# Kernel optimization log

Hardware: AMD Instinct MI355X
Metric: run time of the kernel (lower is better)

Reference implementation:

```python
import jax, jax.numpy as jnp
import numpy as np
import math

B, M, C, H = 4, 2048, 512, 8
DQK = C // 4 // H  # 16 per-head query/key dim


def setup_inputs() -> dict:
    key = jax.random.key(0)
    ks = jax.random.split(key, 8)
    s = 0.02
    return {
        "x": jax.random.normal(ks[0], (B, M, C), dtype=jnp.float32),
        "mask": jax.random.randint(ks[1], (B, M), 0, 2, dtype=jnp.int32),
        "Wq": jax.random.normal(ks[2], (C, C // 4), dtype=jnp.float32) * s,
        "bq": jnp.zeros((C // 4,), dtype=jnp.float32),
        "Wk": jax.random.normal(ks[3], (C, C // 4), dtype=jnp.float32) * s,
        "bk": jnp.zeros((C // 4,), dtype=jnp.float32),
        "Wv": jax.random.normal(ks[4], (C, C), dtype=jnp.float32) * s,
        "bv": jnp.zeros((C,), dtype=jnp.float32),
        "gamma": jnp.ones((1,), dtype=jnp.float32),
    }


def reference(x, mask, Wq, bq, Wk, bk, Wv, bv, gamma):
    b, m, c = x.shape
    # projections, split heads: q/k -> (B, H, M, DQK), v -> (B, H, M, C//H)
    q = (x @ Wq + bq).reshape(b, m, H, -1).transpose(0, 2, 1, 3)
    k = (x @ Wk + bk).reshape(b, m, H, -1).transpose(0, 2, 1, 3)
    v = (x @ Wv + bv).reshape(b, m, H, -1).transpose(0, 2, 1, 3)
    scale = 1.0 / math.sqrt(q.shape[-1])
    scores = jnp.einsum('bhmd,bhnd->bhmn', q, k) * scale
    beta = jax.nn.softmax(jax.nn.relu(scores), axis=-1)  # act='relu' pre-softmax
    # att_drop = 0.0 -> identity
    mf = mask.astype(x.dtype)[:, None, None, :]  # (B,1,1,M)
    beta = beta * mf
    beta = beta / (beta.sum(-1, keepdims=True) + 1e-12)
    o = gamma * jnp.einsum('bhmn,bhnd->bhmd', beta, v)  # (B,H,M,C//H)
    return o.transpose(0, 2, 1, 3).reshape(b, m, c)
```

## Files before the change

### kernel.cpp

```cpp
#include <hip/hip_runtime.h>
#include <hip/hip_bf16.h>

#define MSEQ 2048

typedef __attribute__((ext_vector_type(8))) short short8;
typedef __attribute__((ext_vector_type(4))) float f32x4;

static __device__ __forceinline__ short bf16b(float f) {
    __hip_bfloat16 h = __float2bfloat16(f);
    return *reinterpret_cast<short*>(&h);
}

static __device__ __forceinline__ unsigned int pk2(float a, float b) {
    float2 f2; f2.x = a; f2.y = b;
    __hip_bfloat162 p = __float22bfloat162_rn(f2);
    return *reinterpret_cast<unsigned int*>(&p);
}

static __device__ __forceinline__ void gl_lds16(const void* g, void* l) {
    __builtin_amdgcn_global_load_lds(
        (const __attribute__((address_space(1))) unsigned int*)g,
        (__attribute__((address_space(3))) unsigned int*)l, 16, 0, 0);
}

__global__ __launch_bounds__(256) void wtrans_kernel(
    const float* __restrict__ Wq, const float* __restrict__ Wk,
    const float* __restrict__ Wv, unsigned short* __restrict__ WT)
{
    const int nt = blockIdx.x;
    const int kt = blockIdx.y;
    const int t  = threadIdx.x;
    const int k0 = kt*64;

    const float* W; int ld, n0;
    if (nt < 2)      { W = Wq; ld = 128; n0 = nt*64; }
    else if (nt < 4) { W = Wk; ld = 128; n0 = (nt-2)*64; }
    else             { W = Wv; ld = 512; n0 = (nt-4)*64; }

    __shared__ unsigned short Ts[64*72];

    #pragma unroll
    for (int s = 0; s < 4; ++s) {
        const int lin = s*256 + t;
        const int krow = lin >> 4, ng = lin & 15;
        const float4 v = *(const float4*)(W + (size_t)(k0+krow)*ld + n0 + ng*4);
        Ts[(ng*4+0)*72 + krow] = (unsigned short)bf16b(v.x);
        Ts[(ng*4+1)*72 + krow] = (unsigned short)bf16b(v.y);
        Ts[(ng*4+2)*72 + krow] = (unsigned short)bf16b(v.z);
        Ts[(ng*4+3)*72 + krow] = (unsigned short)bf16b(v.w);
    }
    __syncthreads();
    #pragma unroll
    for (int s = 0; s < 2; ++s) {
        const int lin = s*256 + t;
        const int nrow = lin >> 3, kg = lin & 7;
        *(short8*)(WT + (size_t)(nt*64 + nrow)*512 + k0 + kg*8) = *(const short8*)&Ts[nrow*72 + kg*8];
    }
}

__global__ __launch_bounds__(256, 2) void proj_mfma(
    const float* __restrict__ x, const unsigned short* __restrict__ WT,
    const float* __restrict__ bq, const float* __restrict__ bk, const float* __restrict__ bv,
    unsigned short* __restrict__ Qh, unsigned short* __restrict__ Kh, unsigned short* __restrict__ Vf)
{
    const int nt = blockIdx.x;
    const int r0 = blockIdx.y * 128;
    const int n0 = nt * 128;
    const int t = threadIdx.x, w = t >> 6, lane = t & 63, l15 = lane & 15, quad = lane >> 4;
    const int wqh = w >> 1, wch = w & 1;

    __shared__ short smem[128*136];
    short* As = smem;
    short* Bs = smem + 128*32;

    f32x4 acc[4][4];
    #pragma unroll
    for (int i = 0; i < 4; ++i)
        #pragma unroll
        for (int j = 0; j < 4; ++j) acc[i][j] = {0.f,0.f,0.f,0.f};

    const int brow = lane >> 2, bkg = lane & 3;

    for (int kk = 0; kk < 512; kk += 32) {
        #pragma unroll
        for (int s = 0; s < 2; ++s)
            gl_lds16(WT + (size_t)(n0 + w*32 + s*16 + brow)*512 + kk + bkg*8,
                     Bs + (w*32 + s*16)*32);
        #pragma unroll
        for (int s = 0; s < 4; ++s) {
            const int idx = s*256 + t;
            const int row = idx >> 3, cg = idx & 7;
            const float4 v = *(const float4*)(x + (size_t)(r0+row)*512 + kk + cg*4);
            uint2 uu; uu.x = pk2(v.x, v.y); uu.y = pk2(v.z, v.w);
            *(uint2*)&As[row*32 + cg*4] = uu;
        }
        __syncthreads();
        short8 Af[4], Bf[4];
        #pragma unroll
        for (int i = 0; i < 4; ++i) Af[i] = *(const short8*)&As[(wqh*64 + i*16 + l15)*32 + quad*8];
        #pragma unroll
        for (int j = 0; j < 4; ++j) Bf[j] = *(const short8*)&Bs[(wch*64 + j*16 + l15)*32 + quad*8];
        #pragma unroll
        for (int i = 0; i < 4; ++i)
            #pragma unroll
            for (int j = 0; j < 4; ++j)
                acc[i][j] = __builtin_amdgcn_mfma_f32_16x16x32_bf16(Af[i], Bf[j], acc[i][j], 0, 0, 0);
        __syncthreads();
    }

    const float* bias = (nt == 0) ? bq : (nt == 1) ? bk : (bv + (nt-2)*128);
    float bj[4];
    #pragma unroll
    for (int j = 0; j < 4; ++j) bj[j] = bias[wch*64 + j*16 + l15];

    short* Ts = smem;
    if (nt < 2) {
        #pragma unroll
        for (int i = 0; i < 4; ++i)
            #pragma unroll
            for (int j = 0; j < 4; ++j)
                #pragma unroll
                for (int r = 0; r < 4; ++r)
                    Ts[(wqh*64 + i*16 + quad*4 + r)*136 + wch*64 + j*16 + l15] =
                        bf16b(acc[i][j][r] + bj[j]);
    } else {
        #pragma unroll
        for (int i = 0; i < 4; ++i)
            #pragma unroll
            for (int j = 0; j < 4; ++j)
                #pragma unroll
                for (int r = 0; r < 4; ++r)
                    Ts[(wch*64 + j*16 + l15)*136 + wqh*64 + i*16 + quad*4 + r] =
                        bf16b(acc[i][j][r] + bj[j]);
    }
    __syncthreads();

    const int b = r0 >> 11, key0 = r0 & 2047;
    if (nt < 2) {
        unsigned short* Out = (nt == 0) ? Qh : Kh;
        #pragma unroll
        for (int s = 0; s < 8; ++s) {
            const int lin = s*256 + t, row = lin >> 4, seg = lin & 15;
            const int h = seg >> 1, dh = seg & 1;
            *(short8*)(Out + ((size_t)(b*8 + h)*MSEQ + key0 + row)*16 + dh*8) =
                *(const short8*)&Ts[row*136 + seg*8];
        }
    } else {
        const int kt0 = key0 >> 6, h0 = (nt-2)*2;
        #pragma unroll
        for (int s = 0; s < 8; ++s) {
            const int lin = s*256 + t;
            const int lane_ = lin & 63, kh = (lin>>6)&1, ci = (lin>>7)&1;
            const int chh = (lin>>8)&1, kt_l = (lin>>9)&1, h_l = (lin>>10)&1;
            const int l15_ = lane_ & 15, quad_ = lane_ >> 4;
            const int ch_local  = h_l*64 + (chh*2+ci)*16 + l15_;
            const int key_local = kt_l*64 + kh*32 + quad_*8;
            const size_t addr = ((((((size_t)(b*8 + h0 + h_l)*32 + kt0 + kt_l)*2 + chh)*2 + ci)*2 + kh)*512)
                                + lane_*8;
            *(short8*)(Vf + addr) = *(const short8*)&Ts[ch_local*136 + key_local];
        }
    }
}

__global__ __launch_bounds__(256, 4) void attn_mfma(
    const unsigned short* __restrict__ Qh, const unsigned short* __restrict__ Kh,
    const unsigned short* __restrict__ Vf, const int* __restrict__ mask,
    const float* __restrict__ gamma, float* __restrict__ out)
{
    const int m0 = blockIdx.x * 64;
    const int bh = blockIdx.y;
    const int b  = bh >> 3, h = bh & 7;
    const int t  = threadIdx.x;
    const int wave = t >> 6, lane = t & 63, l15 = lane & 15, quad = lane >> 4;
    const int qh = wave >> 1, chh = wave & 1;

    __shared__ short Ws[2*64*68];
    __shared__ float wsl[4*64];
    __shared__ float wsums[64];

    const short8 zz = {0,0,0,0,0,0,0,0};

    const unsigned short* Qrow = Qh + (size_t)(b*8 + h)*MSEQ*16;
    const unsigned short* Krow = Kh + (size_t)(b*8 + h)*MSEQ*16;
    const unsigned short* Vbh  = Vf + (size_t)(b*8 + h)*32*4096;

    short8 qfrag[4];
    #pragma unroll
    for (int c = 0; c < 4; ++c)
        qfrag[c] = (quad < 2)
            ? *(const short8*)(Qrow + (size_t)(m0 + c*16 + l15)*16 + quad*8)
            : zz;

    f32x4 acc[2][2] = {{{0.f,0.f,0.f,0.f},{0.f,0.f,0.f,0.f}},
                       {{0.f,0.f,0.f,0.f},{0.f,0.f,0.f,0.f}}};
    float wsum_acc[4] = {0.f,0.f,0.f,0.f};

    for (int kt = 0; kt < 32; ++kt) {
        const int kn0 = kt*64;
        short* Wp = Ws + (kt & 1)*64*68;

        const short8 kfrag = (quad < 2)
            ? *(const short8*)(Krow + (size_t)(kn0 + wave*16 + l15)*16 + quad*8)
            : zz;
        const int4 mi = *(const int4*)(mask + b*MSEQ + kn0 + wave*16 + quad*4);
        const float mk[4] = {(float)mi.x, (float)mi.y, (float)mi.z, (float)mi.w};

        #pragma unroll
        for (int c = 0; c < 4; ++c) {
            f32x4 s = {0.f,0.f,0.f,0.f};
            s = __builtin_amdgcn_mfma_f32_16x16x32_bf16(kfrag, qfrag[c], s, 0, 0, 0);
            float w0 = mk[0] * __expf(fmaxf(0.25f*s[0], 0.f));
            float w1 = mk[1] * __expf(fmaxf(0.25f*s[1], 0.f));
            float w2 = mk[2] * __expf(fmaxf(0.25f*s[2], 0.f));
            float w3 = mk[3] * __expf(fmaxf(0.25f*s[3], 0.f));
            uint2 uu; uu.x = pk2(w0, w1); uu.y = pk2(w2, w3);
            *(uint2*)&Wp[(c*16 + l15)*68 + wave*16 + quad*4] = uu;
            wsum_acc[c] += (w0 + w1) + (w2 + w3);
        }

        short8 Bf[2][2];
        #pragma unroll
        for (int ci = 0; ci < 2; ++ci)
            #pragma unroll
            for (int kh = 0; kh < 2; ++kh)
                Bf[ci][kh] = *(const short8*)(Vbh
                    + (size_t)((((kt*2 + chh)*2 + ci)*2 + kh))*512 + lane*8);

        __syncthreads();

        short8 Af[2][2];
        #pragma unroll
        for (int si = 0; si < 2; ++si)
            #pragma unroll
            for (int kh = 0; kh < 2; ++kh)
                Af[si][kh] = *(const short8*)&Wp[((qh*2+si)*16 + l15)*68 + kh*32 + quad*8];
        #pragma unroll
        for (int si = 0; si < 2; ++si)
            #pragma unroll
            for (int ci = 0; ci < 2; ++ci)
                #pragma unroll
                for (int kh = 0; kh < 2; ++kh)
                    acc[si][ci] = __builtin_amdgcn_mfma_f32_16x16x32_bf16(
                        Af[si][kh], Bf[ci][kh], acc[si][ci], 0, 0, 0);
    }

    #pragma unroll
    for (int c = 0; c < 4; ++c) {
        float v = wsum_acc[c];
        v += __shfl_xor(v, 16, 64);
        v += __shfl_xor(v, 32, 64);
        if (quad == 0) wsl[wave*64 + c*16 + l15] = v;
    }
    __syncthreads();
    if (t < 64) wsums[t] = (wsl[t] + wsl[64+t]) + (wsl[128+t] + wsl[192+t]);
    __syncthreads();

    const float g = gamma[0];
    #pragma unroll
    for (int si = 0; si < 2; ++si) {
        #pragma unroll
        for (int r = 0; r < 4; ++r) {
            const int row = qh*32 + si*16 + quad*4 + r;
            const float inv = g / fmaxf(wsums[row], 1e-20f);
            #pragma unroll
            for (int ci = 0; ci < 2; ++ci) {
                const int col = chh*32 + ci*16 + l15;
                out[(size_t)(b*MSEQ + m0 + row)*512 + h*64 + col] = acc[si][ci][r] * inv;
            }
        }
    }
}

extern "C" void kernel_launch(void* const* d_in, const int* in_sizes, int n_in,
                              void* d_out, int out_size, void* d_ws, size_t ws_size,
                              hipStream_t stream) {
    const float* x     = (const float*)d_in[0];
    const int*   mask  = (const int*)  d_in[1];
    const float* Wq    = (const float*)d_in[2];
    const float* bq    = (const float*)d_in[3];
    const float* Wk    = (const float*)d_in[4];
    const float* bk    = (const float*)d_in[5];
    const float* Wv    = (const float*)d_in[6];
    const float* bv    = (const float*)d_in[7];
    const float* gamma = (const float*)d_in[8];
    float* outp = (float*)d_out;

    unsigned short* WT = (unsigned short*)d_ws;
    unsigned short* Qh = WT + (size_t)768*512;
    unsigned short* Kh = Qh + (size_t)8192*128;
    unsigned short* Vf = Kh + (size_t)8192*128;

    wtrans_kernel<<<dim3(12, 8), 256, 0, stream>>>(Wq, Wk, Wv, WT);
    proj_mfma<<<dim3(6, 64), 256, 0, stream>>>(x, WT, bq, bk, bv, Qh, Kh, Vf);
    attn_mfma<<<dim3(32, 32), 256, 0, stream>>>(Qh, Kh, Vf, mask, gamma, outp);
}
```

Measured before the change: 174.1 us.

## Halve projection row tile and prefetch next K/V/mask tiles in attention

```diff
diff --git a/kernel.cpp b/kernel.cpp
--- a/kernel.cpp
+++ b/kernel.cpp
@@ -58,24 +58,24 @@
     }
 }
 
-__global__ __launch_bounds__(256, 2) void proj_mfma(
+__global__ __launch_bounds__(256, 4) void proj_mfma(
     const float* __restrict__ x, const unsigned short* __restrict__ WT,
     const float* __restrict__ bq, const float* __restrict__ bk, const float* __restrict__ bv,
     unsigned short* __restrict__ Qh, unsigned short* __restrict__ Kh, unsigned short* __restrict__ Vf)
 {
     const int nt = blockIdx.x;
-    const int r0 = blockIdx.y * 128;
+    const int r0 = blockIdx.y * 64;
     const int n0 = nt * 128;
     const int t = threadIdx.x, w = t >> 6, lane = t & 63, l15 = lane & 15, quad = lane >> 4;
     const int wqh = w >> 1, wch = w & 1;
 
-    __shared__ short smem[128*136];
+    __shared__ short smem[128*72];
     short* As = smem;
-    short* Bs = smem + 128*32;
-
-    f32x4 acc[4][4];
-    #pragma unroll
-    for (int i = 0; i < 4; ++i)
+    short* Bs = smem + 64*32;
+
+    f32x4 acc[2][4];
+    #pragma unroll
+    for (int i = 0; i < 2; ++i)
         #pragma unroll
         for (int j = 0; j < 4; ++j) acc[i][j] = {0.f,0.f,0.f,0.f};
 
@@ -87,7 +87,7 @@
             gl_lds16(WT + (size_t)(n0 + w*32 + s*16 + brow)*512 + kk + bkg*8,
                      Bs + (w*32 + s*16)*32);
         #pragma unroll
-        for (int s = 0; s < 4; ++s) {
+        for (int s = 0; s < 2; ++s) {
             const int idx = s*256 + t;
             const int row = idx >> 3, cg = idx & 7;
             const float4 v = *(const float4*)(x + (size_t)(r0+row)*512 + kk + cg*4);
@@ -95,13 +95,13 @@
             *(uint2*)&As[row*32 + cg*4] = uu;
         }
         __syncthreads();
-        short8 Af[4], Bf[4];
-        #pragma unroll
-        for (int i = 0; i < 4; ++i) Af[i] = *(const short8*)&As[(wqh*64 + i*16 + l15)*32 + quad*8];
+        short8 Af[2], Bf[4];
+        #pragma unroll
+        for (int i = 0; i < 2; ++i) Af[i] = *(const short8*)&As[(wqh*32 + i*16 + l15)*32 + quad*8];
         #pragma unroll
         for (int j = 0; j < 4; ++j) Bf[j] = *(const short8*)&Bs[(wch*64 + j*16 + l15)*32 + quad*8];
         #pragma unroll
-        for (int i = 0; i < 4; ++i)
+        for (int i = 0; i < 2; ++i)
             #pragma unroll
             for (int j = 0; j < 4; ++j)
                 acc[i][j] = __builtin_amdgcn_mfma_f32_16x16x32_bf16(Af[i], Bf[j], acc[i][j], 0, 0, 0);
@@ -113,51 +113,49 @@
     #pragma unroll
     for (int j = 0; j < 4; ++j) bj[j] = bias[wch*64 + j*16 + l15];
 
-    short* Ts = smem;
+    const int b = r0 >> 11, key0 = r0 & 2047;
     if (nt < 2) {
-        #pragma unroll
-        for (int i = 0; i < 4; ++i)
+        short* Ts = smem;
+        #pragma unroll
+        for (int i = 0; i < 2; ++i)
             #pragma unroll
             for (int j = 0; j < 4; ++j)
                 #pragma unroll
                 for (int r = 0; r < 4; ++r)
-                    Ts[(wqh*64 + i*16 + quad*4 + r)*136 + wch*64 + j*16 + l15] =
+                    Ts[(wqh*32 + i*16 + quad*4 + r)*136 + wch*64 + j*16 + l15] =
                         bf16b(acc[i][j][r] + bj[j]);
-    } else {
-        #pragma unroll
-        for (int i = 0; i < 4; ++i)
-            #pragma unroll
-            for (int j = 0; j < 4; ++j)
-                #pragma unroll
-                for (int r = 0; r < 4; ++r)
-                    Ts[(wch*64 + j*16 + l15)*136 + wqh*64 + i*16 + quad*4 + r] =
-                        bf16b(acc[i][j][r] + bj[j]);
-    }
-    __syncthreads();
-
-    const int b = r0 >> 11, key0 = r0 & 2047;
-    if (nt < 2) {
+        __syncthreads();
         unsigned short* Out = (nt == 0) ? Qh : Kh;
         #pragma unroll
-        for (int s = 0; s < 8; ++s) {
+        for (int s = 0; s < 4; ++s) {
             const int lin = s*256 + t, row = lin >> 4, seg = lin & 15;
             const int h = seg >> 1, dh = seg & 1;
             *(short8*)(Out + ((size_t)(b*8 + h)*MSEQ + key0 + row)*16 + dh*8) =
                 *(const short8*)&Ts[row*136 + seg*8];
         }
     } else {
+        short* Ts = smem;
+        #pragma unroll
+        for (int i = 0; i < 2; ++i)
+            #pragma unroll
+            for (int j = 0; j < 4; ++j)
+                #pragma unroll
+                for (int r = 0; r < 4; ++r)
+                    Ts[(wch*64 + j*16 + l15)*72 + wqh*32 + i*16 + quad*4 + r] =
+                        bf16b(acc[i][j][r] + bj[j]);
+        __syncthreads();
         const int kt0 = key0 >> 6, h0 = (nt-2)*2;
         #pragma unroll
-        for (int s = 0; s < 8; ++s) {
+        for (int s = 0; s < 4; ++s) {
             const int lin = s*256 + t;
             const int lane_ = lin & 63, kh = (lin>>6)&1, ci = (lin>>7)&1;
-            const int chh = (lin>>8)&1, kt_l = (lin>>9)&1, h_l = (lin>>10)&1;
+            const int chh = (lin>>8)&1, h_l = (lin>>9)&1;
             const int l15_ = lane_ & 15, quad_ = lane_ >> 4;
             const int ch_local  = h_l*64 + (chh*2+ci)*16 + l15_;
-            const int key_local = kt_l*64 + kh*32 + quad_*8;
-            const size_t addr = ((((((size_t)(b*8 + h0 + h_l)*32 + kt0 + kt_l)*2 + chh)*2 + ci)*2 + kh)*512)
+            const int key_local = kh*32 + quad_*8;
+            const size_t addr = (((((size_t)(b*8 + h0 + h_l)*32 + kt0)*2 + chh)*2 + ci)*2 + kh)*512
                                 + lane_*8;
-            *(short8*)(Vf + addr) = *(const short8*)&Ts[ch_local*136 + key_local];
+            *(short8*)(Vf + addr) = *(const short8*)&Ts[ch_local*72 + key_local];
         }
     }
 }
@@ -183,6 +181,7 @@
     const unsigned short* Qrow = Qh + (size_t)(b*8 + h)*MSEQ*16;
     const unsigned short* Krow = Kh + (size_t)(b*8 + h)*MSEQ*16;
     const unsigned short* Vbh  = Vf + (size_t)(b*8 + h)*32*4096;
+    const int* mrow = mask + b*MSEQ + wave*16 + quad*4;
 
     short8 qfrag[4];
     #pragma unroll
@@ -195,14 +194,39 @@
                        {{0.f,0.f,0.f,0.f},{0.f,0.f,0.f,0.f}}};
     float wsum_acc[4] = {0.f,0.f,0.f,0.f};
 
+    short8 kfrag_n = (quad < 2)
+        ? *(const short8*)(Krow + (size_t)(wave*16 + l15)*16 + quad*8) : zz;
+    int4 mi_n = *(const int4*)(mrow);
+    short8 Bfn[2][2];
+    #pragma unroll
+    for (int ci = 0; ci < 2; ++ci)
+        #pragma unroll
+        for (int kh = 0; kh < 2; ++kh)
+            Bfn[ci][kh] = *(const short8*)(Vbh + (size_t)(((chh*2 + ci)*2 + kh))*512 + lane*8);
+
     for (int kt = 0; kt < 32; ++kt) {
-        const int kn0 = kt*64;
         short* Wp = Ws + (kt & 1)*64*68;
-
-        const short8 kfrag = (quad < 2)
-            ? *(const short8*)(Krow + (size_t)(kn0 + wave*16 + l15)*16 + quad*8)
-            : zz;
-        const int4 mi = *(const int4*)(mask + b*MSEQ + kn0 + wave*16 + quad*4);
+        const short8 kfrag = kfrag_n;
+        const int4 mi = mi_n;
+        short8 Bf[2][2];
+        #pragma unroll
+        for (int ci = 0; ci < 2; ++ci)
+            #pragma unroll
+            for (int kh = 0; kh < 2; ++kh) Bf[ci][kh] = Bfn[ci][kh];
+
+        if (kt < 31) {
+            const int kn1 = (kt+1)*64;
+            kfrag_n = (quad < 2)
+                ? *(const short8*)(Krow + (size_t)(kn1 + wave*16 + l15)*16 + quad*8) : zz;
+            mi_n = *(const int4*)(mrow + kn1);
+            #pragma unroll
+            for (int ci = 0; ci < 2; ++ci)
+                #pragma unroll
+                for (int kh = 0; kh < 2; ++kh)
+                    Bfn[ci][kh] = *(const short8*)(Vbh
+                        + (size_t)((((kt+1)*2 + chh)*2 + ci)*2 + kh)*512 + lane*8);
+        }
+
         const float mk[4] = {(float)mi.x, (float)mi.y, (float)mi.z, (float)mi.w};
 
         #pragma unroll
@@ -217,14 +241,6 @@
             *(uint2*)&Wp[(c*16 + l15)*68 + wave*16 + quad*4] = uu;
             wsum_acc[c] += (w0 + w1) + (w2 + w3);
         }
-
-        short8 Bf[2][2];
-        #pragma unroll
-        for (int ci = 0; ci < 2; ++ci)
-            #pragma unroll
-            for (int kh = 0; kh < 2; ++kh)
-                Bf[ci][kh] = *(const short8*)(Vbh
-                    + (size_t)((((kt*2 + chh)*2 + ci)*2 + kh))*512 + lane*8);
 
         __syncthreads();
 
@@ -291,6 +307,6 @@
     unsigned short* Vf = Kh + (size_t)8192*128;
 
     wtrans_kernel<<<dim3(12, 8), 256, 0, stream>>>(Wq, Wk, Wv, WT);
-    proj_mfma<<<dim3(6, 64), 256, 0, stream>>>(x, WT, bq, bk, bv, Qh, Kh, Vf);
+    proj_mfma<<<dim3(6, 128), 256, 0, stream>>>(x, WT, bq, bk, bv, Qh, Kh, Vf);
     attn_mfma<<<dim3(32, 32), 256, 0, stream>>>(Qh, Kh, Vf, mask, gamma, outp);
 }
```

Measured after the change: 175.9 us. No clear change (+1.0%).
